# Kernel optimization log

Measured on AMD Instinct MI355X. Metric: run time of the kernel, lower is better.

## Reference

```python
import jax, jax.numpy as jnp
import numpy as np

N_EMBED = 1024
HEAD_SIZE = 64


def setup_inputs() -> dict:
    key = jax.random.key(0)
    kx, kk, kq, kv = jax.random.split(key, 4)
    B, T = 8, 2048
    x = jax.random.normal(kx, (B, T, N_EMBED), dtype=jnp.float32)
    # nn.Linear weights, stored as (in, out) so projection is x @ W
    s = 1.0 / np.sqrt(N_EMBED)
    Wk = jax.random.uniform(kk, (N_EMBED, HEAD_SIZE), jnp.float32, -s, s)
    Wq = jax.random.uniform(kq, (N_EMBED, HEAD_SIZE), jnp.float32, -s, s)
    Wv = jax.random.uniform(kv, (N_EMBED, HEAD_SIZE), jnp.float32, -s, s)
    return {"x": x, "Wk": Wk, "Wq": Wq, "Wv": Wv}


def reference(x, Wk, Wq, Wv):
    # x: [B, T, C] with C = n_embed
    C = x.shape[-1]
    k = x @ Wk  # [B, T, H]
    q = x @ Wq  # [B, T, H]
    v = x @ Wv  # [B, T, H]
    # NOTE: original scales by n_embed**-0.5, not head_size**-0.5
    wei = jnp.einsum("bth,bsh->bts", q, k) * (C ** -0.5)  # [B, T, T]
    wei = jax.nn.softmax(wei, axis=-1)
    # dropout = 0.0 (eval mode) -> identity
    out = jnp.einsum("bts,bsh->bth", wei, v)  # [B, T, H]
    return out
```

## Files before the change

### kernel.cpp

```cpp
#include <hip/hip_runtime.h>
#include <stdint.h>


#define B_ 8
#define T_ 2048
#define C_ 1024
#define H_ 64

typedef float f32x4 __attribute__((ext_vector_type(4)));
typedef short s16x8 __attribute__((ext_vector_type(8)));

__device__ __forceinline__ unsigned int rhu16(float f) {
    return (__float_as_uint(f) + 0x8000u) >> 16;
}
__device__ __forceinline__ unsigned int pkbf(float lo, float hi) {
    unsigned int a = __float_as_uint(lo) + 0x8000u;
    unsigned int b = __float_as_uint(hi) + 0x8000u;
    return __builtin_amdgcn_perm(b, a, 0x07060302u);
}
__device__ __forceinline__ void ld_lds16(const void* g, void* l) {
    __builtin_amdgcn_global_load_lds(
        (const __attribute__((address_space(1))) unsigned int*)g,
        (__attribute__((address_space(3))) unsigned int*)l, 16, 0, 0);
}

__global__ __launch_bounds__(256) void wconv(const float* __restrict__ Wk,
        const float* __restrict__ Wq, const float* __restrict__ Wv,
        unsigned short* __restrict__ Wt) {
    __shared__ float ls[64 * 65];
    const int bx = blockIdx.x, t = threadIdx.x;
    const int mat = bx >> 4, c0 = (bx & 15) << 6;
    const float* W = (mat == 0) ? Wk : ((mat == 1) ? Wq : Wv);
    const float sc = (mat == 1) ? 0.03125f : 1.0f;
    #pragma unroll
    for (int k = 0; k < 4; k++) {
        int i = t + (k << 8);
        int cr = i >> 4, hq = (i & 15) << 2;
        float4 v = *reinterpret_cast<const float4*>(&W[(size_t)(c0 + cr) * H_ + hq]);
        ls[cr * 65 + hq + 0] = v.x; ls[cr * 65 + hq + 1] = v.y;
        ls[cr * 65 + hq + 2] = v.z; ls[cr * 65 + hq + 3] = v.w;
    }
    __syncthreads();
    #pragma unroll
    for (int k = 0; k < 4; k++) {
        int i = t + (k << 8);
        int h = i >> 4, cq = (i & 15) << 2;
        float a = ls[(cq + 0) * 65 + h] * sc, b = ls[(cq + 1) * 65 + h] * sc;
        float c = ls[(cq + 2) * 65 + h] * sc, d = ls[(cq + 3) * 65 + h] * sc;
        uint2 o; o.x = pkbf(a, b); o.y = pkbf(c, d);
        *reinterpret_cast<uint2*>(&Wt[(size_t)(mat * 64 + h) * C_ + c0 + cq]) = o;
    }
}

__global__ __launch_bounds__(256, 2) void qkv(const float* __restrict__ x,
        const unsigned short* __restrict__ Wt,
        unsigned short* __restrict__ kb, unsigned short* __restrict__ qb,
        unsigned short* __restrict__ vtb) {
    __shared__ __align__(16) char smem[65536];
    char* xb = smem;
    char* wb = smem + 16384;

    const int t = threadIdx.x, lane = t & 63, w = t >> 6;
    const int l15 = lane & 15, quad = lane >> 4;
    const int bx = blockIdx.x;
    const int bb = bx >> 6;
    const int mt = ((bx & 7) << 3) | ((bx >> 3) & 7);
    const int m0 = bb * T_ + mt * 32;
    const int colb = w * 48;

    size_t xg[2]; int xl[2];
    #pragma unroll
    for (int n = 0; n < 2; n++) {
        int id = w * 2 + n, rg = id >> 2, j = id & 3;
        xg[n] = (size_t)(m0 + rg * 16 + l15) * C_ + j * 16 + quad * 4;
        xl[n] = id * 1024 + lane * 16;
    }
    size_t wg[6]; int wl[6];
    #pragma unroll
    for (int n = 0; n < 6; n++) {
        int g = w * 6 + n;
        wg[n] = (size_t)(g * 8 + (lane & 7)) * C_ + (lane >> 3) * 8;
        wl[n] = g * 1024 + lane * 16;
    }

    #pragma unroll
    for (int n = 0; n < 2; n++) ld_lds16(x + xg[n], xb + xl[n]);
    #pragma unroll
    for (int n = 0; n < 6; n++) ld_lds16(Wt + wg[n], wb + wl[n]);
    __syncthreads();

    f32x4 acc[2][3];
    #pragma unroll
    for (int rt = 0; rt < 2; rt++)
        #pragma unroll
        for (int ct = 0; ct < 3; ct++)
            #pragma unroll
            for (int j = 0; j < 4; j++) acc[rt][ct][j] = 0.0f;

    #pragma unroll
    for (int i = 0; i < 16; i++) {
        const int cb = i & 1;
        const float* xc = (const float*)(xb + cb * 8192);
        const unsigned short* wc = (const unsigned short*)(wb + cb * 24576);

        float4 xr[2][2][2];
        #pragma unroll
        for (int rt = 0; rt < 2; rt++)
            #pragma unroll
            for (int ks = 0; ks < 2; ks++)
                #pragma unroll
                for (int h = 0; h < 2; h++) {
                    int c = ks * 32 + quad * 8 + h * 4;
                    int j = c >> 4, u = (c & 15) >> 2;
                    xr[rt][ks][h] = *reinterpret_cast<const float4*>(
                        xc + (rt * 4 + j) * 256 + u * 64 + l15 * 4);
                }
        s16x8 wfr[3][2];
        #pragma unroll
        for (int ct = 0; ct < 3; ct++)
            #pragma unroll
            for (int ks = 0; ks < 2; ks++) {
                int col = colb + ct * 16 + l15;
                wfr[ct][ks] = *reinterpret_cast<const s16x8*>(
                    wc + (col >> 3) * 512 + ((4 * ks + quad) * 8 + (col & 7)) * 8);
            }

        if (i < 15) {
            const int c1 = (i + 1) * 64;
            char* xn = xb + (cb ^ 1) * 8192;
            char* wn = wb + (cb ^ 1) * 24576;
            #pragma unroll
            for (int n = 0; n < 2; n++) ld_lds16(x + xg[n] + c1, xn + xl[n]);
            #pragma unroll
            for (int n = 0; n < 6; n++) ld_lds16(Wt + wg[n] + c1, wn + wl[n]);
        }

        s16x8 af[2][2];
        #pragma unroll
        for (int rt = 0; rt < 2; rt++)
            #pragma unroll
            for (int ks = 0; ks < 2; ks++) {
                const float4 a = xr[rt][ks][0], b = xr[rt][ks][1];
                uint4 pk;
                pk.x = pkbf(a.x, a.y); pk.y = pkbf(a.z, a.w);
                pk.z = pkbf(b.x, b.y); pk.w = pkbf(b.z, b.w);
                af[rt][ks] = *reinterpret_cast<s16x8*>(&pk);
            }
        #pragma unroll
        for (int ks = 0; ks < 2; ks++)
            #pragma unroll
            for (int rt = 0; rt < 2; rt++)
                #pragma unroll
                for (int ct = 0; ct < 3; ct++)
                    acc[rt][ct] = __builtin_amdgcn_mfma_f32_16x16x32_bf16(
                        af[rt][ks], wfr[ct][ks], acc[rt][ct], 0, 0, 0);
        __syncthreads();
    }

    #pragma unroll
    for (int ct = 0; ct < 3; ct++) {
        int cbv = colb + ct * 16;
        int sel = cbv >> 6;
        int h = (cbv & 63) + l15;
        #pragma unroll
        for (int rt = 0; rt < 2; rt++) {
            int row0 = m0 + rt * 16 + quad * 4;
            if (sel < 2) {
                unsigned short* dst = sel ? qb : kb;
                #pragma unroll
                for (int r = 0; r < 4; r++)
                    dst[(size_t)(row0 + r) * H_ + h] = (unsigned short)rhu16(acc[rt][ct][r]);
            } else {
                int tt = row0 - bb * T_;
                uint2 pk;
                pk.x = pkbf(acc[rt][ct][0], acc[rt][ct][1]);
                pk.y = pkbf(acc[rt][ct][2], acc[rt][ct][3]);
                *reinterpret_cast<uint2*>(&vtb[((size_t)bb * H_ + h) * T_ + tt]) = pk;
            }
        }
    }
}

__global__ __launch_bounds__(256, 2) void attn(
        const unsigned short* __restrict__ qb,
        const unsigned short* __restrict__ kb,
        const unsigned short* __restrict__ vtb,
        float* __restrict__ out) {
    __shared__ __align__(16) char smem[25728];

    const int t = threadIdx.x, lane = t & 63, w = t >> 6;
    const int l15 = lane & 15, quad = lane >> 4;
    const int bb = blockIdx.x & 7;
    const int q0 = (blockIdx.x >> 3) << 5;
    const size_t kbase = (size_t)bb * T_ * H_;
    unsigned short* Pw = (unsigned short*)(smem + w * 4608);

    s16x8 qf[2][2];
    #pragma unroll
    for (int rt = 0; rt < 2; rt++)
        #pragma unroll
        for (int ks = 0; ks < 2; ks++)
            qf[rt][ks] = *reinterpret_cast<const s16x8*>(
                &qb[kbase + (size_t)(q0 + rt * 16 + l15) * H_ + ks * 32 + quad * 8]);

    const int sw = w << 9;
    const unsigned short* kq = kb + kbase + (size_t)(sw + l15) * H_ + quad * 8;
    const unsigned short* vq[4];
    #pragma unroll
    for (int ht = 0; ht < 4; ht++)
        vq[ht] = vtb + ((size_t)bb * H_ + ht * 16 + l15) * T_ + sw + quad * 8;

    f32x4 oacc[2][4];
    #pragma unroll
    for (int rt = 0; rt < 2; rt++)
        #pragma unroll
        for (int ht = 0; ht < 4; ht++)
            #pragma unroll
            for (int j = 0; j < 4; j++) oacc[rt][ht][j] = 0.0f;
    float l_run[2] = {0.0f, 0.0f};
    const f32x4 z4 = {0.0f, 0.0f, 0.0f, 0.0f};

    for (int it = 0; it < 8; it++) {
        s16x8 kf[4][2], vf[2][4];
        #pragma unroll
        for (int st = 0; st < 4; st++)
            #pragma unroll
            for (int ks = 0; ks < 2; ks++)
                kf[st][ks] = *reinterpret_cast<const s16x8*>(
                    kq + (size_t)(it * 64 + st * 16) * H_ + ks * 32);
        #pragma unroll
        for (int ks2 = 0; ks2 < 2; ks2++)
            #pragma unroll
            for (int ht = 0; ht < 4; ht++)
                vf[ks2][ht] = *reinterpret_cast<const s16x8*>(
                    vq[ht] + it * 64 + ks2 * 32);

        f32x4 sacc[2][4];
        #pragma unroll
        for (int rt = 0; rt < 2; rt++)
            #pragma unroll
            for (int st = 0; st < 4; st++) {
                f32x4 s0v = __builtin_amdgcn_mfma_f32_16x16x32_bf16(
                    kf[st][0], qf[rt][0], z4, 0, 0, 0);
                sacc[rt][st] = __builtin_amdgcn_mfma_f32_16x16x32_bf16(
                    kf[st][1], qf[rt][1], s0v, 0, 0, 0);
            }

        #pragma unroll
        for (int rt = 0; rt < 2; rt++) {
            float ls = 0.0f;
            #pragma unroll
            for (int st = 0; st < 4; st++) {
                float p0 = __expf(sacc[rt][st][0]);
                float p1 = __expf(sacc[rt][st][1]);
                float p2 = __expf(sacc[rt][st][2]);
                float p3 = __expf(sacc[rt][st][3]);
                ls += (p0 + p1) + (p2 + p3);
                uint2 pk; pk.x = pkbf(p0, p1); pk.y = pkbf(p2, p3);
                *reinterpret_cast<uint2*>(
                    &Pw[(rt * 16 + l15) * 72 + st * 16 + quad * 4]) = pk;
            }
            l_run[rt] += ls;
        }

        #pragma unroll
        for (int rt = 0; rt < 2; rt++)
            #pragma unroll
            for (int ks2 = 0; ks2 < 2; ks2++) {
                s16x8 pf = *reinterpret_cast<const s16x8*>(
                    &Pw[(rt * 16 + l15) * 72 + ks2 * 32 + quad * 8]);
                #pragma unroll
                for (int ht = 0; ht < 4; ht++)
                    oacc[rt][ht] = __builtin_amdgcn_mfma_f32_16x16x32_bf16(
                        pf, vf[ks2][ht], oacc[rt][ht], 0, 0, 0);
            }
    }

    #pragma unroll
    for (int rt = 0; rt < 2; rt++) {
        l_run[rt] += __shfl_xor(l_run[rt], 16);
        l_run[rt] += __shfl_xor(l_run[rt], 32);
    }

    __syncthreads();
    float* Osf = (float*)smem;
    float* Ls  = (float*)smem + 3 * 32 * 66;
    if (w > 0) {
        int wi = w - 1;
        #pragma unroll
        for (int rt = 0; rt < 2; rt++) {
            if (quad == 0) Ls[wi * 32 + rt * 16 + l15] = l_run[rt];
            #pragma unroll
            for (int ht = 0; ht < 4; ht++)
                #pragma unroll
                for (int r = 0; r < 4; r++)
                    Osf[wi * 2112 + (rt * 16 + quad * 4 + r) * 66 + ht * 16 + l15] = oacc[rt][ht][r];
        }
    }
    __syncthreads();
    if (w == 0) {
        #pragma unroll
        for (int rt = 0; rt < 2; rt++)
            #pragma unroll
            for (int r = 0; r < 4; r++) {
                int row = rt * 16 + quad * 4 + r;
                float lt = __shfl(l_run[rt], quad * 4 + r)
                         + Ls[0 * 32 + row] + Ls[1 * 32 + row] + Ls[2 * 32 + row];
                float inv = 1.0f / lt;
                #pragma unroll
                for (int ht = 0; ht < 4; ht++) {
                    float o = oacc[rt][ht][r]
                            + Osf[0 * 2112 + row * 66 + ht * 16 + l15]
                            + Osf[1 * 2112 + row * 66 + ht * 16 + l15]
                            + Osf[2 * 2112 + row * 66 + ht * 16 + l15];
                    out[kbase + (size_t)(q0 + row) * H_ + ht * 16 + l15] = o * inv;
                }
            }
    }
}

extern "C" void kernel_launch(void* const* d_in, const int* in_sizes, int n_in,
                              void* d_out, int out_size, void* d_ws, size_t ws_size,
                              hipStream_t stream) {
    const float* x  = (const float*)d_in[0];
    const float* Wk = (const float*)d_in[1];
    const float* Wq = (const float*)d_in[2];
    const float* Wv = (const float*)d_in[3];

    unsigned short* kb  = (unsigned short*)d_ws;
    unsigned short* qbf = kb  + (size_t)B_ * T_ * H_;
    unsigned short* vtb = qbf + (size_t)B_ * T_ * H_;
    unsigned short* Wt  = (unsigned short*)d_out;

    wconv<<<48,  256, 0, stream>>>(Wk, Wq, Wv, Wt);
    qkv  <<<512, 256, 0, stream>>>(x, Wt, kb, qbf, vtb);
    attn <<<512, 256, 0, stream>>>(qbf, kb, vtb, (float*)d_out);
}
```

Before: 152.1 us.

## Load QKV projection operands directly from global memory instead of LDS staging

```diff
diff --git a/kernel.cpp b/kernel.cpp
--- a/kernel.cpp
+++ b/kernel.cpp
@@ -17,11 +17,6 @@
     unsigned int a = __float_as_uint(lo) + 0x8000u;
     unsigned int b = __float_as_uint(hi) + 0x8000u;
     return __builtin_amdgcn_perm(b, a, 0x07060302u);
-}
-__device__ __forceinline__ void ld_lds16(const void* g, void* l) {
-    __builtin_amdgcn_global_load_lds(
-        (const __attribute__((address_space(1))) unsigned int*)g,
-        (__attribute__((address_space(3))) unsigned int*)l, 16, 0, 0);
 }
 
 __global__ __launch_bounds__(256) void wconv(const float* __restrict__ Wk,
@@ -56,38 +51,22 @@
         const unsigned short* __restrict__ Wt,
         unsigned short* __restrict__ kb, unsigned short* __restrict__ qb,
         unsigned short* __restrict__ vtb) {
-    __shared__ __align__(16) char smem[65536];
-    char* xb = smem;
-    char* wb = smem + 16384;
-
     const int t = threadIdx.x, lane = t & 63, w = t >> 6;
     const int l15 = lane & 15, quad = lane >> 4;
     const int bx = blockIdx.x;
     const int bb = bx >> 6;
-    const int mt = ((bx & 7) << 3) | ((bx >> 3) & 7);
+    const int mt = bx & 63;
     const int m0 = bb * T_ + mt * 32;
     const int colb = w * 48;
 
-    size_t xg[2]; int xl[2];
-    #pragma unroll
-    for (int n = 0; n < 2; n++) {
-        int id = w * 2 + n, rg = id >> 2, j = id & 3;
-        xg[n] = (size_t)(m0 + rg * 16 + l15) * C_ + j * 16 + quad * 4;
-        xl[n] = id * 1024 + lane * 16;
-    }
-    size_t wg[6]; int wl[6];
-    #pragma unroll
-    for (int n = 0; n < 6; n++) {
-        int g = w * 6 + n;
-        wg[n] = (size_t)(g * 8 + (lane & 7)) * C_ + (lane >> 3) * 8;
-        wl[n] = g * 1024 + lane * 16;
-    }
-
-    #pragma unroll
-    for (int n = 0; n < 2; n++) ld_lds16(x + xg[n], xb + xl[n]);
-    #pragma unroll
-    for (int n = 0; n < 6; n++) ld_lds16(Wt + wg[n], wb + wl[n]);
-    __syncthreads();
+    const float* xa[2];
+    #pragma unroll
+    for (int rt = 0; rt < 2; rt++)
+        xa[rt] = x + (size_t)(m0 + rt * 16 + l15) * C_ + quad * 8;
+    const unsigned short* wa[3];
+    #pragma unroll
+    for (int ct = 0; ct < 3; ct++)
+        wa[ct] = Wt + (size_t)(colb + ct * 16 + l15) * C_ + quad * 8;
 
     f32x4 acc[2][3];
     #pragma unroll
@@ -99,53 +78,29 @@
 
     #pragma unroll
     for (int i = 0; i < 16; i++) {
-        const int cb = i & 1;
-        const float* xc = (const float*)(xb + cb * 8192);
-        const unsigned short* wc = (const unsigned short*)(wb + cb * 24576);
-
-        float4 xr[2][2][2];
-        #pragma unroll
-        for (int rt = 0; rt < 2; rt++)
+        const int k0 = i * 64;
+
+        s16x8 wfr[3][2];
+        #pragma unroll
+        for (int ct = 0; ct < 3; ct++)
             #pragma unroll
             for (int ks = 0; ks < 2; ks++)
-                #pragma unroll
-                for (int h = 0; h < 2; h++) {
-                    int c = ks * 32 + quad * 8 + h * 4;
-                    int j = c >> 4, u = (c & 15) >> 2;
-                    xr[rt][ks][h] = *reinterpret_cast<const float4*>(
-                        xc + (rt * 4 + j) * 256 + u * 64 + l15 * 4);
-                }
-        s16x8 wfr[3][2];
-        #pragma unroll
-        for (int ct = 0; ct < 3; ct++)
+                wfr[ct][ks] = *reinterpret_cast<const s16x8*>(wa[ct] + k0 + ks * 32);
+
+        s16x8 af[2][2];
+        #pragma unroll
+        for (int rt = 0; rt < 2; rt++)
             #pragma unroll
             for (int ks = 0; ks < 2; ks++) {
-                int col = colb + ct * 16 + l15;
-                wfr[ct][ks] = *reinterpret_cast<const s16x8*>(
-                    wc + (col >> 3) * 512 + ((4 * ks + quad) * 8 + (col & 7)) * 8);
-            }
-
-        if (i < 15) {
-            const int c1 = (i + 1) * 64;
-            char* xn = xb + (cb ^ 1) * 8192;
-            char* wn = wb + (cb ^ 1) * 24576;
-            #pragma unroll
-            for (int n = 0; n < 2; n++) ld_lds16(x + xg[n] + c1, xn + xl[n]);
-            #pragma unroll
-            for (int n = 0; n < 6; n++) ld_lds16(Wt + wg[n] + c1, wn + wl[n]);
-        }
-
-        s16x8 af[2][2];
-        #pragma unroll
-        for (int rt = 0; rt < 2; rt++)
-            #pragma unroll
-            for (int ks = 0; ks < 2; ks++) {
-                const float4 a = xr[rt][ks][0], b = xr[rt][ks][1];
+                const float* p = xa[rt] + k0 + ks * 32;
+                float4 a = *reinterpret_cast<const float4*>(p);
+                float4 b = *reinterpret_cast<const float4*>(p + 4);
                 uint4 pk;
                 pk.x = pkbf(a.x, a.y); pk.y = pkbf(a.z, a.w);
                 pk.z = pkbf(b.x, b.y); pk.w = pkbf(b.z, b.w);
                 af[rt][ks] = *reinterpret_cast<s16x8*>(&pk);
             }
+
         #pragma unroll
         for (int ks = 0; ks < 2; ks++)
             #pragma unroll
@@ -154,7 +109,6 @@
                 for (int ct = 0; ct < 3; ct++)
                     acc[rt][ct] = __builtin_amdgcn_mfma_f32_16x16x32_bf16(
                         af[rt][ks], wfr[ct][ks], acc[rt][ct], 0, 0, 0);
-        __syncthreads();
     }
 
     #pragma unroll
```

New measurement: 189.0 us. +24.2%, slower.

## Split qkv projection work across 8 waves per block instead of 4

Applied to the files above, without the earlier changes.

```diff
diff --git a/kernel.cpp b/kernel.cpp
--- a/kernel.cpp
+++ b/kernel.cpp
@@ -52,7 +52,8 @@
     }
 }
 
-__global__ __launch_bounds__(256, 2) void qkv(const float* __restrict__ x,
+__global__ __launch_bounds__(512) __attribute__((amdgpu_waves_per_eu(4, 4)))
+void qkv(const float* __restrict__ x,
         const unsigned short* __restrict__ Wt,
         unsigned short* __restrict__ kb, unsigned short* __restrict__ qb,
         unsigned short* __restrict__ vtb) {
@@ -64,57 +65,52 @@
     const int l15 = lane & 15, quad = lane >> 4;
     const int bx = blockIdx.x;
     const int bb = bx >> 6;
-    const int mt = ((bx & 7) << 3) | ((bx >> 3) & 7);
+    const int mt = bx & 63;
     const int m0 = bb * T_ + mt * 32;
-    const int colb = w * 48;
-
-    size_t xg[2]; int xl[2];
-    #pragma unroll
-    for (int n = 0; n < 2; n++) {
-        int id = w * 2 + n, rg = id >> 2, j = id & 3;
-        xg[n] = (size_t)(m0 + rg * 16 + l15) * C_ + j * 16 + quad * 4;
-        xl[n] = id * 1024 + lane * 16;
-    }
-    size_t wg[6]; int wl[6];
-    #pragma unroll
-    for (int n = 0; n < 6; n++) {
-        int g = w * 6 + n;
+    const int wr = w >> 2;
+    const int colb = (w & 3) * 48;
+
+    size_t xg; int xl;
+    {
+        int rg = w >> 2, j = w & 3;
+        xg = (size_t)(m0 + rg * 16 + l15) * C_ + j * 16 + quad * 4;
+        xl = w * 1024 + lane * 16;
+    }
+    size_t wg[3]; int wl[3];
+    #pragma unroll
+    for (int n = 0; n < 3; n++) {
+        int g = w * 3 + n;
         wg[n] = (size_t)(g * 8 + (lane & 7)) * C_ + (lane >> 3) * 8;
         wl[n] = g * 1024 + lane * 16;
     }
 
-    #pragma unroll
-    for (int n = 0; n < 2; n++) ld_lds16(x + xg[n], xb + xl[n]);
-    #pragma unroll
-    for (int n = 0; n < 6; n++) ld_lds16(Wt + wg[n], wb + wl[n]);
+    ld_lds16(x + xg, xb + xl);
+    #pragma unroll
+    for (int n = 0; n < 3; n++) ld_lds16(Wt + wg[n], wb + wl[n]);
     __syncthreads();
 
-    f32x4 acc[2][3];
-    #pragma unroll
-    for (int rt = 0; rt < 2; rt++)
-        #pragma unroll
-        for (int ct = 0; ct < 3; ct++)
-            #pragma unroll
-            for (int j = 0; j < 4; j++) acc[rt][ct][j] = 0.0f;
+    f32x4 acc[3];
+    #pragma unroll
+    for (int ct = 0; ct < 3; ct++)
+        #pragma unroll
+        for (int j = 0; j < 4; j++) acc[ct][j] = 0.0f;
 
     #pragma unroll
     for (int i = 0; i < 16; i++) {
         const int cb = i & 1;
         const float* xc = (const float*)(xb + cb * 8192);
-        const unsigned short* wc = (const unsigned short*)(wb + cb * 24576);
-
-        float4 xr[2][2][2];
-        #pragma unroll
-        for (int rt = 0; rt < 2; rt++)
-            #pragma unroll
-            for (int ks = 0; ks < 2; ks++)
-                #pragma unroll
-                for (int h = 0; h < 2; h++) {
-                    int c = ks * 32 + quad * 8 + h * 4;
-                    int j = c >> 4, u = (c & 15) >> 2;
-                    xr[rt][ks][h] = *reinterpret_cast<const float4*>(
-                        xc + (rt * 4 + j) * 256 + u * 64 + l15 * 4);
-                }
+        const unsigned short* wcp = (const unsigned short*)(wb + cb * 24576);
+
+        float4 xr[2][2];
+        #pragma unroll
+        for (int ks = 0; ks < 2; ks++)
+            #pragma unroll
+            for (int h = 0; h < 2; h++) {
+                int c = ks * 32 + quad * 8 + h * 4;
+                int j = c >> 4, u = (c & 15) >> 2;
+                xr[ks][h] = *reinterpret_cast<const float4*>(
+                    xc + (wr * 4 + j) * 256 + u * 64 + l15 * 4);
+            }
         s16x8 wfr[3][2];
         #pragma unroll
         for (int ct = 0; ct < 3; ct++)
@@ -122,38 +118,33 @@
             for (int ks = 0; ks < 2; ks++) {
                 int col = colb + ct * 16 + l15;
                 wfr[ct][ks] = *reinterpret_cast<const s16x8*>(
-                    wc + (col >> 3) * 512 + ((4 * ks + quad) * 8 + (col & 7)) * 8);
+                    wcp + (col >> 3) * 512 + ((4 * ks + quad) * 8 + (col & 7)) * 8);
             }
 
         if (i < 15) {
             const int c1 = (i + 1) * 64;
             char* xn = xb + (cb ^ 1) * 8192;
             char* wn = wb + (cb ^ 1) * 24576;
-            #pragma unroll
-            for (int n = 0; n < 2; n++) ld_lds16(x + xg[n] + c1, xn + xl[n]);
-            #pragma unroll
-            for (int n = 0; n < 6; n++) ld_lds16(Wt + wg[n] + c1, wn + wl[n]);
-        }
-
-        s16x8 af[2][2];
-        #pragma unroll
-        for (int rt = 0; rt < 2; rt++)
-            #pragma unroll
-            for (int ks = 0; ks < 2; ks++) {
-                const float4 a = xr[rt][ks][0], b = xr[rt][ks][1];
-                uint4 pk;
-                pk.x = pkbf(a.x, a.y); pk.y = pkbf(a.z, a.w);
-                pk.z = pkbf(b.x, b.y); pk.w = pkbf(b.z, b.w);
-                af[rt][ks] = *reinterpret_cast<s16x8*>(&pk);
-            }
+            ld_lds16(x + xg + c1, xn + xl);
+            #pragma unroll
+            for (int n = 0; n < 3; n++) ld_lds16(Wt + wg[n] + c1, wn + wl[n]);
+        }
+
+        s16x8 af[2];
+        #pragma unroll
+        for (int ks = 0; ks < 2; ks++) {
+            const float4 a = xr[ks][0], b = xr[ks][1];
+            uint4 pk;
+            pk.x = pkbf(a.x, a.y); pk.y = pkbf(a.z, a.w);
+            pk.z = pkbf(b.x, b.y); pk.w = pkbf(b.z, b.w);
+            af[ks] = *reinterpret_cast<s16x8*>(&pk);
+        }
         #pragma unroll
         for (int ks = 0; ks < 2; ks++)
             #pragma unroll
-            for (int rt = 0; rt < 2; rt++)
-                #pragma unroll
-                for (int ct = 0; ct < 3; ct++)
-                    acc[rt][ct] = __builtin_amdgcn_mfma_f32_16x16x32_bf16(
-                        af[rt][ks], wfr[ct][ks], acc[rt][ct], 0, 0, 0);
+            for (int ct = 0; ct < 3; ct++)
+                acc[ct] = __builtin_amdgcn_mfma_f32_16x16x32_bf16(
+                    af[ks], wfr[ct][ks], acc[ct], 0, 0, 0);
         __syncthreads();
     }
 
@@ -162,21 +153,18 @@
         int cbv = colb + ct * 16;
         int sel = cbv >> 6;
         int h = (cbv & 63) + l15;
-        #pragma unroll
-        for (int rt = 0; rt < 2; rt++) {
-            int row0 = m0 + rt * 16 + quad * 4;
-            if (sel < 2) {
-                unsigned short* dst = sel ? qb : kb;
-                #pragma unroll
-                for (int r = 0; r < 4; r++)
-                    dst[(size_t)(row0 + r) * H_ + h] = (unsigned short)rhu16(acc[rt][ct][r]);
-            } else {
-                int tt = row0 - bb * T_;
-                uint2 pk;
-                pk.x = pkbf(acc[rt][ct][0], acc[rt][ct][1]);
-                pk.y = pkbf(acc[rt][ct][2], acc[rt][ct][3]);
-                *reinterpret_cast<uint2*>(&vtb[((size_t)bb * H_ + h) * T_ + tt]) = pk;
-            }
+        int row0 = m0 + wr * 16 + quad * 4;
+        if (sel < 2) {
+            unsigned short* dst = sel ? qb : kb;
+            #pragma unroll
+            for (int r = 0; r < 4; r++)
+                dst[(size_t)(row0 + r) * H_ + h] = (unsigned short)rhu16(acc[ct][r]);
+        } else {
+            int tt = row0 - bb * T_;
+            uint2 pk;
+            pk.x = pkbf(acc[ct][0], acc[ct][1]);
+            pk.y = pkbf(acc[ct][2], acc[ct][3]);
+            *reinterpret_cast<uint2*>(&vtb[((size_t)bb * H_ + h) * T_ + tt]) = pk;
         }
     }
 }
@@ -333,6 +321,6 @@
     unsigned short* Wt  = (unsigned short*)d_out;
 
     wconv<<<48,  256, 0, stream>>>(Wk, Wq, Wv, Wt);
-    qkv  <<<512, 256, 0, stream>>>(x, Wt, kb, qbf, vtb);
+    qkv  <<<512, 512, 0, stream>>>(x, Wt, kb, qbf, vtb);
     attn <<<512, 256, 0, stream>>>(qbf, kb, vtb, (float*)d_out);
 }
```

Result: no change. 152.0 us (-0.1%).

## Widen QKV projection tile to 64 rows with 512-thread blocks sharing weights

Applied to the files above, without the earlier changes.

```diff
diff --git a/kernel.cpp b/kernel.cpp
--- a/kernel.cpp
+++ b/kernel.cpp
@@ -52,21 +52,20 @@
     }
 }
 
-__global__ __launch_bounds__(256, 2) void qkv(const float* __restrict__ x,
+__global__ __launch_bounds__(512) __attribute__((amdgpu_waves_per_eu(2)))
+void qkv(const float* __restrict__ x,
         const unsigned short* __restrict__ Wt,
         unsigned short* __restrict__ kb, unsigned short* __restrict__ qb,
         unsigned short* __restrict__ vtb) {
-    __shared__ __align__(16) char smem[65536];
-    char* xb = smem;
-    char* wb = smem + 16384;
-
+    __shared__ __align__(16) char smem[81920];
     const int t = threadIdx.x, lane = t & 63, w = t >> 6;
     const int l15 = lane & 15, quad = lane >> 4;
     const int bx = blockIdx.x;
-    const int bb = bx >> 6;
-    const int mt = ((bx & 7) << 3) | ((bx >> 3) & 7);
-    const int m0 = bb * T_ + mt * 32;
-    const int colb = w * 48;
+    const int bb = bx >> 5;
+    const int mt = bx & 31;
+    const int m0 = bb * T_ + mt * 64;
+    const int wr = w >> 2;
+    const int colb = (w & 3) * 48;
 
     size_t xg[2]; int xl[2];
     #pragma unroll
@@ -75,18 +74,18 @@
         xg[n] = (size_t)(m0 + rg * 16 + l15) * C_ + j * 16 + quad * 4;
         xl[n] = id * 1024 + lane * 16;
     }
-    size_t wg[6]; int wl[6];
-    #pragma unroll
-    for (int n = 0; n < 6; n++) {
-        int g = w * 6 + n;
+    size_t wg[3]; int wl[3];
+    #pragma unroll
+    for (int n = 0; n < 3; n++) {
+        int g = w * 3 + n;
         wg[n] = (size_t)(g * 8 + (lane & 7)) * C_ + (lane >> 3) * 8;
-        wl[n] = g * 1024 + lane * 16;
-    }
-
-    #pragma unroll
-    for (int n = 0; n < 2; n++) ld_lds16(x + xg[n], xb + xl[n]);
-    #pragma unroll
-    for (int n = 0; n < 6; n++) ld_lds16(Wt + wg[n], wb + wl[n]);
+        wl[n] = 16384 + g * 1024 + lane * 16;
+    }
+
+    #pragma unroll
+    for (int n = 0; n < 2; n++) ld_lds16(x + xg[n], smem + xl[n]);
+    #pragma unroll
+    for (int n = 0; n < 3; n++) ld_lds16(Wt + wg[n], smem + wl[n]);
     __syncthreads();
 
     f32x4 acc[2][3];
@@ -100,8 +99,9 @@
     #pragma unroll
     for (int i = 0; i < 16; i++) {
         const int cb = i & 1;
-        const float* xc = (const float*)(xb + cb * 8192);
-        const unsigned short* wc = (const unsigned short*)(wb + cb * 24576);
+        const char* cur = smem + cb * 40960;
+        const float* xc = (const float*)cur;
+        const unsigned short* wcp = (const unsigned short*)(cur + 16384);
 
         float4 xr[2][2][2];
         #pragma unroll
@@ -112,8 +112,9 @@
                 for (int h = 0; h < 2; h++) {
                     int c = ks * 32 + quad * 8 + h * 4;
                     int j = c >> 4, u = (c & 15) >> 2;
+                    int rg = wr * 2 + rt;
                     xr[rt][ks][h] = *reinterpret_cast<const float4*>(
-                        xc + (rt * 4 + j) * 256 + u * 64 + l15 * 4);
+                        xc + (rg * 4 + j) * 256 + u * 64 + l15 * 4);
                 }
         s16x8 wfr[3][2];
         #pragma unroll
@@ -122,17 +123,16 @@
             for (int ks = 0; ks < 2; ks++) {
                 int col = colb + ct * 16 + l15;
                 wfr[ct][ks] = *reinterpret_cast<const s16x8*>(
-                    wc + (col >> 3) * 512 + ((4 * ks + quad) * 8 + (col & 7)) * 8);
+                    wcp + (col >> 3) * 512 + ((4 * ks + quad) * 8 + (col & 7)) * 8);
             }
 
         if (i < 15) {
             const int c1 = (i + 1) * 64;
-            char* xn = xb + (cb ^ 1) * 8192;
-            char* wn = wb + (cb ^ 1) * 24576;
-            #pragma unroll
-            for (int n = 0; n < 2; n++) ld_lds16(x + xg[n] + c1, xn + xl[n]);
-            #pragma unroll
-            for (int n = 0; n < 6; n++) ld_lds16(Wt + wg[n] + c1, wn + wl[n]);
+            char* nxt = smem + (cb ^ 1) * 40960;
+            #pragma unroll
+            for (int n = 0; n < 2; n++) ld_lds16(x + xg[n] + c1, nxt + xl[n]);
+            #pragma unroll
+            for (int n = 0; n < 3; n++) ld_lds16(Wt + wg[n] + c1, nxt + wl[n]);
         }
 
         s16x8 af[2][2];
@@ -164,7 +164,7 @@
         int h = (cbv & 63) + l15;
         #pragma unroll
         for (int rt = 0; rt < 2; rt++) {
-            int row0 = m0 + rt * 16 + quad * 4;
+            int row0 = m0 + (wr * 2 + rt) * 16 + quad * 4;
             if (sel < 2) {
                 unsigned short* dst = sel ? qb : kb;
                 #pragma unroll
@@ -333,6 +333,6 @@
     unsigned short* Wt  = (unsigned short*)d_out;
 
     wconv<<<48,  256, 0, stream>>>(Wk, Wq, Wv, Wt);
-    qkv  <<<512, 256, 0, stream>>>(x, Wt, kb, qbf, vtb);
+    qkv  <<<256, 512, 0, stream>>>(x, Wt, kb, qbf, vtb);
     attn <<<512, 256, 0, stream>>>(qbf, kb, vtb, (float*)d_out);
 }
```

Result: no change. 154.4 us (+1.5%).
